# Kernel tuning notes

Hardware: AMD Instinct MI355X
Metric: run time of the kernel (lower is better)

The kernel has to match this reference:

```python
import jax, jax.numpy as jnp
import numpy as np

N_NODES = 50000
N_EDGES = 400000
N_GRAPHS = 128
IN_DIM = 768
HID = 128
N_CLASSES = 11
BN_EPS = 1e-5


def _sage_conv(x, src, dst, Wl, bl, Wr):
    # PyG SAGEConv (aggr='mean'): out = lin_l(mean_{j->i} x_j) + lin_r(x_i)
    # messages flow src -> dst; nodes with no in-edges get a zero aggregate.
    n = x.shape[0]
    deg = jax.ops.segment_sum(jnp.ones_like(dst, x.dtype), dst, num_segments=n)
    agg = jax.ops.segment_sum(x[src], dst, num_segments=n)  # [N, d] gather+scatter
    agg = agg / jnp.maximum(deg, 1.0)[:, None]
    return agg @ Wl.T + bl + x @ Wr.T


def _batch_norm(x, gamma, beta):
    # training-mode BatchNorm1d: biased batch statistics over the node axis
    m = jnp.mean(x, axis=0)
    v = jnp.var(x, axis=0)
    return (x - m) * jax.lax.rsqrt(v + BN_EPS) * gamma + beta


def setup_inputs() -> dict:
    key = jax.random.key(0)
    ks = jax.random.split(key, 16)
    x = jax.random.normal(ks[0], (N_NODES, IN_DIM), dtype=jnp.float32)
    edge_index = jax.random.randint(ks[1], (2, N_EDGES), 0, N_NODES, dtype=jnp.int32)
    batch = jnp.sort(jax.random.randint(ks[2], (N_NODES,), 0, N_GRAPHS, dtype=jnp.int32))

    def lin_w(k, out_d, in_d):
        return jax.random.normal(k, (out_d, in_d), dtype=jnp.float32) * (1.0 / np.sqrt(in_d))

    params = {
        'W1l': lin_w(ks[3], HID, IN_DIM), 'b1': jnp.zeros((HID,), jnp.float32),
        'W1r': lin_w(ks[4], HID, IN_DIM),
        'g1': jnp.ones((HID,), jnp.float32), 'be1': jnp.zeros((HID,), jnp.float32),
        'W2l': lin_w(ks[5], HID, HID), 'b2': jnp.zeros((HID,), jnp.float32),
        'W2r': lin_w(ks[6], HID, HID),
        'g2': jnp.ones((HID,), jnp.float32), 'be2': jnp.zeros((HID,), jnp.float32),
        'W3l': lin_w(ks[7], HID, HID), 'b3': jnp.zeros((HID,), jnp.float32),
        'W3r': lin_w(ks[8], HID, HID),
        'g3': jnp.ones((HID,), jnp.float32), 'be3': jnp.zeros((HID,), jnp.float32),
        'Wlin': lin_w(ks[9], N_CLASSES, HID), 'blin': jnp.zeros((N_CLASSES,), jnp.float32),
    }
    return {'x': x, 'edge_index': edge_index, 'batch': batch, **params}


def reference(x, edge_index, batch,
              W1l, b1, W1r, g1, be1,
              W2l, b2, W2r, g2, be2,
              W3l, b3, W3r, g3, be3,
              Wlin, blin):
    src, dst = edge_index[0], edge_index[1]
    h = jax.nn.relu(_batch_norm(_sage_conv(x, src, dst, W1l, b1, W1r), g1, be1))
    h = jax.nn.relu(_batch_norm(_sage_conv(h, src, dst, W2l, b2, W2r), g2, be2))
    h = _batch_norm(_sage_conv(h, src, dst, W3l, b3, W3r), g3, be3)
    # global_max_pool over graph ids
    pooled = jax.ops.segment_max(h, batch, num_segments=N_GRAPHS)  # [G, HID]
    # dropout is identity at inference
    return pooled @ Wlin.T + blin  # [G, 11]
```

## Files before the change

### kernel.cpp

```cpp
#include <hip/hip_runtime.h>

#define N_NODESC 50000
#define N_EDGESC 400000
#define N_GRAPHSC 128
#define IN_DIMC 768
#define HIDC 128
#define NCLSC 11
#define BN_EPSC 1e-5f
#define NB_AGG 8
#define NREP 64
#define SCAN_NB ((N_NODESC + 255) / 256)

typedef __bf16 bf16_t;
typedef __bf16 bf16x2 __attribute__((ext_vector_type(2)));
typedef __bf16 bf16x8 __attribute__((ext_vector_type(8)));
typedef float f32x4 __attribute__((ext_vector_type(4)));

typedef __attribute__((address_space(1))) void glb_void;
typedef __attribute__((address_space(3))) void lds_void;

__device__ __forceinline__ void cp16(const void* g, void* l) {
    __builtin_amdgcn_global_load_lds((glb_void*)g, (lds_void*)l, 16, 0, 0);
}

__device__ __forceinline__ f32x4 mfma_16x16x32_bf16(bf16x8 a, bf16x8 b, f32x4 c) {
    return __builtin_amdgcn_mfma_f32_16x16x32_bf16(a, b, c, 0, 0, 0);
}

template<int MODE, int KC>
__global__ __launch_bounds__(256) void gemm_kernel(const void* __restrict__ Av,
                                                   const bf16_t* __restrict__ Wb,
                                                   const float* __restrict__ stats,
                                                   const float* __restrict__ g,
                                                   const float* __restrict__ be,
                                                   bf16_t* __restrict__ Cl,
                                                   bf16_t* __restrict__ Cr,
                                                   int M)
{
    constexpr int NK   = KC / 32;
    constexpr int ASZ  = 8192;
    constexpr int BSZ  = 8192;
    constexpr int SCSZ = (MODE == 1) ? 1024 : 16;
    __shared__ __align__(16) unsigned char smem[3 * ASZ + 3 * BSZ + SCSZ];
    unsigned char* Asm = smem;
    unsigned char* Bsm = smem + 3 * ASZ;
    float* scS = (float*)(smem + 3 * ASZ + 3 * BSZ);

    const int bid  = blockIdx.x;
    const int p    = ((bid >> 4) << 3) + (bid & 7);
    const int half = (bid >> 3) & 1;
    if (p * 128 >= M) return;
    const int m0 = p * 128;

    const int t    = threadIdx.x;
    const int wid  = t >> 6;
    const int lane = t & 63;
    const int wm   = (wid >> 1) * 64;
    const int wn   = (wid & 1) * 64;
    const int l16  = lane & 15;
    const int quad = lane >> 4;

    const char* bSrc[2]; int bDst[2];
#pragma unroll
    for (int s = 0; s < 2; s++) {
        int L = (s * 4 + wid) * 64 + lane;
        int r = L >> 2;
        int c = (L & 3) ^ ((r >> 1) & 3);
        bSrc[s] = (const char*)(Wb + (size_t)(half * 128 + r) * KC + c * 8);
        bDst[s] = (s * 4 + wid) * 1024;
    }

    const char* aSrc[2]; int aDst[2];
    if constexpr (MODE == 1) {
#pragma unroll
        for (int s = 0; s < 2; s++) {
            int L = (s * 4 + wid) * 64 + lane;
            int r = L >> 2;
            int c = (L & 3) ^ ((r >> 1) & 3);
            int row = m0 + r; if (row > M - 1) row = M - 1;
            aSrc[s] = (const char*)Av + ((size_t)row * KC + (size_t)c * 8) * 2;
            aDst[s] = (s * 4 + wid) * 1024;
        }
    }

    const int rL = (wid << 5) + (lane >> 1);
    int rAg = m0 + rL; if (rAg > M - 1) rAg = M - 1;
    const int hA = lane & 1;
    const float* aG = (const float*)Av + (size_t)rAg * KC + hA * 16;
    const int cA0 = hA * 2;
    const int wb0 = rL * 64 + (((cA0)     ^ ((rL >> 1) & 3)) << 4);
    const int wb1 = rL * 64 + (((cA0 + 1) ^ ((rL >> 1) & 3)) << 4);

    int aOff[4], bOff[4];
#pragma unroll
    for (int i = 0; i < 4; i++) {
        int ra = wm + i * 16 + l16;
        aOff[i] = ra * 64 + ((quad ^ ((ra >> 1) & 3)) << 4);
        int rb = wn + i * 16 + l16;
        bOff[i] = rb * 64 + ((quad ^ ((rb >> 1) & 3)) << 4);
    }

    if (MODE == 1) {
        if (t < HIDC) {
            float sum = 0.f, sumsq = 0.f;
            for (int r = 0; r < NREP; r++) {
                sum   += stats[r * 256 + t];
                sumsq += stats[r * 256 + HIDC + t];
            }
            float invM = 1.0f / (float)M;
            float mean = sum * invM;
            float var  = sumsq * invM - mean * mean;
            float s = rsqrtf(var + BN_EPSC) * g[t];
            scS[t] = s;
            scS[HIDC + t] = be[t] - mean * s;
        }
        __syncthreads();
    }

    f32x4 acc[4][4] = {};

#define ALD(IT, G0, G1, G2, G3) { \
        const float4* _p = (const float4*)(aG + (size_t)(IT) * 32); \
        G0 = _p[0]; G1 = _p[1]; G2 = _p[2]; G3 = _p[3]; }
#define CVTW(G0, G1, G2, G3, DST) { \
        bf16x8 _w0, _w1; \
        _w0[0]=(bf16_t)G0.x; _w0[1]=(bf16_t)G0.y; _w0[2]=(bf16_t)G0.z; _w0[3]=(bf16_t)G0.w; \
        _w0[4]=(bf16_t)G1.x; _w0[5]=(bf16_t)G1.y; _w0[6]=(bf16_t)G1.z; _w0[7]=(bf16_t)G1.w; \
        _w1[0]=(bf16_t)G2.x; _w1[1]=(bf16_t)G2.y; _w1[2]=(bf16_t)G2.z; _w1[3]=(bf16_t)G2.w; \
        _w1[4]=(bf16_t)G3.x; _w1[5]=(bf16_t)G3.y; _w1[6]=(bf16_t)G3.z; _w1[7]=(bf16_t)G3.w; \
        *(bf16x8*)((DST) + wb0) = _w0; *(bf16x8*)((DST) + wb1) = _w1; }

    if constexpr (MODE == 0) {
        float4 gaA0, gaA1, gaA2, gaA3;
        float4 gaB0, gaB1, gaB2, gaB3;

        ALD(0, gaA0, gaA1, gaA2, gaA3);
#pragma unroll
        for (int s = 0; s < 2; s++) cp16(bSrc[s], Bsm + bDst[s]);
        ALD(1, gaB0, gaB1, gaB2, gaB3);
#pragma unroll
        for (int s = 0; s < 2; s++) cp16(bSrc[s] + 64, Bsm + BSZ + bDst[s]);
        CVTW(gaA0, gaA1, gaA2, gaA3, Asm);

        for (int it = 0; it < NK; ++it) {
            if (it + 1 < NK) asm volatile("s_waitcnt vmcnt(6) lgkmcnt(0)" ::: "memory");
            else             asm volatile("s_waitcnt vmcnt(0) lgkmcnt(0)" ::: "memory");
            asm volatile("s_barrier" ::: "memory");

            if (it + 2 < NK) {
                const size_t kb = (size_t)(it + 2) * 64;
                const int nb = (it + 2) % 3;
#pragma unroll
                for (int s = 0; s < 2; s++) cp16(bSrc[s] + kb, Bsm + nb * BSZ + bDst[s]);
                if ((it & 1) == 0) { ALD(it + 2, gaA0, gaA1, gaA2, gaA3); }
                else               { ALD(it + 2, gaB0, gaB1, gaB2, gaB3); }
            }
            if (it + 1 < NK) {
                unsigned char* Ad = Asm + ((it + 1) % 3) * ASZ;
                if ((it & 1) == 0) { CVTW(gaB0, gaB1, gaB2, gaB3, Ad); }
                else               { CVTW(gaA0, gaA1, gaA2, gaA3, Ad); }
            }

            const unsigned char* Ab = Asm + (it % 3) * ASZ;
            const unsigned char* Bb = Bsm + (it % 3) * BSZ;
            bf16x8 af[4], bfr[4];
#pragma unroll
            for (int i = 0; i < 4; i++)
                af[i] = *(const bf16x8*)(Ab + aOff[i]);
#pragma unroll
            for (int j = 0; j < 4; j++)
                bfr[j] = *(const bf16x8*)(Bb + bOff[j]);
#pragma unroll
            for (int i = 0; i < 4; i++)
#pragma unroll
                for (int j = 0; j < 4; j++)
                    acc[i][j] = mfma_16x16x32_bf16(af[i], bfr[j], acc[i][j]);
        }
    } else {
#pragma unroll
        for (int s = 0; s < 2; s++) cp16(aSrc[s], Asm + aDst[s]);
#pragma unroll
        for (int s = 0; s < 2; s++) cp16(bSrc[s], Bsm + bDst[s]);
#pragma unroll
        for (int s = 0; s < 2; s++) cp16(aSrc[s] + 64, Asm + ASZ + aDst[s]);
#pragma unroll
        for (int s = 0; s < 2; s++) cp16(bSrc[s] + 64, Bsm + BSZ + bDst[s]);

        for (int it = 0; it < NK; ++it) {
            if (it + 2 < NK) {
                const size_t kb2 = (size_t)(it + 2) * 64;
                const int nb = (it + 2) % 3;
#pragma unroll
                for (int s = 0; s < 2; s++) cp16(aSrc[s] + kb2, Asm + nb * ASZ + aDst[s]);
#pragma unroll
                for (int s = 0; s < 2; s++) cp16(bSrc[s] + kb2, Bsm + nb * BSZ + bDst[s]);
                asm volatile("s_waitcnt vmcnt(8)" ::: "memory");
            } else if (it + 1 < NK) {
                asm volatile("s_waitcnt vmcnt(4)" ::: "memory");
            } else {
                asm volatile("s_waitcnt vmcnt(0)" ::: "memory");
            }
            asm volatile("s_barrier" ::: "memory");

            const unsigned char* Ab = Asm + (it % 3) * ASZ;
            const unsigned char* Bb = Bsm + (it % 3) * BSZ;
            bf16x8 af[4], bfr[4];
            float4 s0 = *(const float4*)&scS[it * 32 + quad * 8];
            float4 s1 = *(const float4*)&scS[it * 32 + quad * 8 + 4];
            float4 h0 = *(const float4*)&scS[HIDC + it * 32 + quad * 8];
            float4 h1 = *(const float4*)&scS[HIDC + it * 32 + quad * 8 + 4];
            float ss[8] = {s0.x, s0.y, s0.z, s0.w, s1.x, s1.y, s1.z, s1.w};
            float hh[8] = {h0.x, h0.y, h0.z, h0.w, h1.x, h1.y, h1.z, h1.w};
#pragma unroll
            for (int i = 0; i < 4; i++) {
                bf16x8 raw = *(const bf16x8*)(Ab + aOff[i]);
#pragma unroll
                for (int e = 0; e < 8; e++)
                    af[i][e] = (bf16_t)fmaxf(fmaf((float)raw[e], ss[e], hh[e]), 0.0f);
            }
#pragma unroll
            for (int j = 0; j < 4; j++)
                bfr[j] = *(const bf16x8*)(Bb + bOff[j]);
#pragma unroll
            for (int i = 0; i < 4; i++)
#pragma unroll
                for (int j = 0; j < 4; j++)
                    acc[i][j] = mfma_16x16x32_bf16(af[i], bfr[j], acc[i][j]);

            asm volatile("s_barrier" ::: "memory");
        }
    }
#undef ALD
#undef CVTW

    bf16_t* C = half ? Cr : Cl;
#pragma unroll
    for (int i = 0; i < 4; i++) {
        int rowb = m0 + wm + i * 16 + quad * 4;
#pragma unroll
        for (int j = 0; j < 4; j++) {
            int colh = wn + j * 16 + l16;
#pragma unroll
            for (int rr = 0; rr < 4; rr++) {
                int row = rowb + rr;
                if (row < M) C[(size_t)row * HIDC + colh] = (bf16_t)acc[i][j][rr];
            }
        }
    }
}

__global__ void init_kernel(const float* __restrict__ W1l, const float* __restrict__ W1r,
                            const float* __restrict__ W2l, const float* __restrict__ W2r,
                            const float* __restrict__ W3l, const float* __restrict__ W3r,
                            bf16_t* __restrict__ Wb1, bf16_t* __restrict__ Wb2,
                            bf16_t* __restrict__ Wb3,
                            int* __restrict__ degi, float* __restrict__ stats)
{
    const int NW1 = 128 * IN_DIMC;
    const int NW2 = 128 * HIDC;
    const int NS  = 3 * NREP * 256;
    int j = blockIdx.x * blockDim.x + threadIdx.x;
    if (j < 2 * NW1) { Wb1[j] = (bf16_t)((j < NW1) ? W1l[j] : W1r[j - NW1]); return; }
    j -= 2 * NW1;
    if (j < 2 * NW2) { Wb2[j] = (bf16_t)((j < NW2) ? W2l[j] : W2r[j - NW2]); return; }
    j -= 2 * NW2;
    if (j < 2 * NW2) { Wb3[j] = (bf16_t)((j < NW2) ? W3l[j] : W3r[j - NW2]); return; }
    j -= 2 * NW2;
    if (j < NS) { stats[j] = 0.0f; return; }
    j -= NS;
    if (j < N_NODESC) degi[j] = 0;
}

__global__ void degi_kernel(const int* __restrict__ ei, int* __restrict__ degi) {
    int e = blockIdx.x * blockDim.x + threadIdx.x;
    if (e < N_EDGESC) atomicAdd(&degi[ei[N_EDGESC + e]], 1);
}

__global__ __launch_bounds__(256) void scan1_kernel(const int* __restrict__ degi,
                                                    int* __restrict__ local,
                                                    int* __restrict__ partials)
{
    __shared__ int tmp[256];
    const int t = threadIdx.x;
    const int i = blockIdx.x * 256 + t;
    int v = (i < N_NODESC) ? degi[i] : 0;
    tmp[t] = v;
    __syncthreads();
    for (int off = 1; off < 256; off <<= 1) {
        int u = (t >= off) ? tmp[t - off] : 0;
        __syncthreads();
        tmp[t] += u;
        __syncthreads();
    }
    if (i < N_NODESC) local[i] = tmp[t] - v;
    if (t == 255) partials[blockIdx.x] = tmp[255];
}

__global__ __launch_bounds__(256) void scan3_kernel(const int* __restrict__ local,
                                                    const int* __restrict__ partials,
                                                    int* __restrict__ rowptr,
                                                    int* __restrict__ cursor)
{
    __shared__ int inc[256];
    __shared__ int orig[256];
    const int t = threadIdx.x;
    int v = (t < SCAN_NB) ? partials[t] : 0;
    inc[t] = v; orig[t] = v;
    __syncthreads();
    for (int off = 1; off < 256; off <<= 1) {
        int u = (t >= off) ? inc[t - off] : 0;
        __syncthreads();
        inc[t] += u;
        __syncthreads();
    }
    const int boff = inc[blockIdx.x] - orig[blockIdx.x];
    const int i = blockIdx.x * 256 + t;
    if (i < N_NODESC) {
        int r = local[i] + boff;
        rowptr[i] = r;
        cursor[i] = r;
    }
    if (i == 0) rowptr[N_NODESC] = N_EDGESC;
}

__global__ void fill_kernel(const int* __restrict__ ei, int* __restrict__ cursor,
                            int* __restrict__ col) {
    int e = blockIdx.x * blockDim.x + threadIdx.x;
    if (e >= N_EDGESC) return;
    int d = ei[N_EDGESC + e];
    int pos = atomicAdd(&cursor[d], 1);
    col[pos] = ei[e];
}

__global__ __launch_bounds__(128) void agg_combine_kernel(const int* __restrict__ rowptr,
                                                          const int* __restrict__ col,
                                                          const bf16_t* __restrict__ Plb,
                                                          const bf16_t* __restrict__ Prb,
                                                          const float* __restrict__ bias,
                                                          bf16_t* __restrict__ Hb,
                                                          float* __restrict__ stats, int M)
{
    const int lane = threadIdx.x & 63;
    const int wv   = threadIdx.x >> 6;
    const int c0   = lane * 2;
    const float b0 = bias[c0], b1v = bias[c0 + 1];
    float s0 = 0.f, s1 = 0.f, q0 = 0.f, q1 = 0.f;
    const int n0 = blockIdx.x * NB_AGG + wv * (NB_AGG / 2);
    for (int rr = 0; rr < NB_AGG / 2; rr++) {
        int n = n0 + rr;
        if (n >= M) break;
        int lo = rowptr[n], hi = rowptr[n + 1];
        float a0 = 0.f, a1 = 0.f;
        for (int e = lo; e < hi; e += 8) {
            int rem = hi - e;
            int idx[8];
#pragma unroll
            for (int j = 0; j < 8; j++) {
                int ee = e + j; if (ee > hi - 1) ee = hi - 1;
                idx[j] = col[ee];
            }
            bf16x2 v[8];
#pragma unroll
            for (int j = 0; j < 8; j++)
                v[j] = *(const bf16x2*)&Plb[(size_t)idx[j] * HIDC + c0];
#pragma unroll
            for (int j = 0; j < 8; j++)
                if (j < rem) { a0 += (float)v[j][0]; a1 += (float)v[j][1]; }
        }
        int d = hi - lo;
        float inv = 1.0f / (float)(d > 0 ? d : 1);
        bf16x2 pr = *(const bf16x2*)&Prb[(size_t)n * HIDC + c0];
        float pre0 = fmaf(a0, inv, b0) + (float)pr[0];
        float pre1 = fmaf(a1, inv, b1v) + (float)pr[1];
        bf16x2 hv; hv[0] = (bf16_t)pre0; hv[1] = (bf16_t)pre1;
        *(bf16x2*)&Hb[(size_t)n * HIDC + c0] = hv;
        s0 += pre0; s1 += pre1; q0 += pre0 * pre0; q1 += pre1 * pre1;
    }
    const int rep = (blockIdx.x * 2 + wv) & (NREP - 1);
    atomicAdd(&stats[rep * 256 + c0], s0);
    atomicAdd(&stats[rep * 256 + c0 + 1], s1);
    atomicAdd(&stats[rep * 256 + HIDC + c0], q0);
    atomicAdd(&stats[rep * 256 + HIDC + c0 + 1], q1);
}

__global__ __launch_bounds__(128) void poolhead_kernel(const bf16_t* __restrict__ Hb,
                                                       const float* __restrict__ stats,
                                                       const float* __restrict__ g,
                                                       const float* __restrict__ be,
                                                       const int* __restrict__ batch,
                                                       const float* __restrict__ Wlin,
                                                       const float* __restrict__ blin,
                                                       float* __restrict__ out, int M)
{
    __shared__ float sp[HIDC];
    int gph = blockIdx.x;
    int c   = threadIdx.x;
    float sum = 0.f, sumsq = 0.f;
    for (int r = 0; r < NREP; r++) {
        sum   += stats[r * 256 + c];
        sumsq += stats[r * 256 + HIDC + c];
    }
    float invM = 1.0f / (float)M;
    float mean = sum * invM;
    float var  = sumsq * invM - mean * mean;
    float s = rsqrtf(var + BN_EPSC) * g[c];
    float h = be[c] - mean * s;

    int lo = 0, hi = M;
    while (lo < hi) { int m = (lo + hi) >> 1; if (batch[m] < gph) lo = m + 1; else hi = m; }
    int lo2 = lo, hi2 = M;
    while (lo2 < hi2) { int m = (lo2 + hi2) >> 1; if (batch[m] < gph + 1) lo2 = m + 1; else hi2 = m; }
    float mx = -INFINITY;
    for (int rr = lo; rr < lo2; rr++)
        mx = fmaxf(mx, fmaf((float)Hb[(size_t)rr * HIDC + c], s, h));
    sp[c] = mx;
    __syncthreads();
    if (c < NCLSC) {
        float acc = blin[c];
        for (int k = 0; k < HIDC; k++) acc += sp[k] * Wlin[c * HIDC + k];
        out[gph * NCLSC + c] = acc;
    }
}

extern "C" void kernel_launch(void* const* d_in, const int* in_sizes, int n_in,
                              void* d_out, int out_size, void* d_ws, size_t ws_size,
                              hipStream_t stream)
{
    const float* x     = (const float*)d_in[0];
    const int*   ei    = (const int*)d_in[1];
    const int*   batch = (const int*)d_in[2];
    const float* W1l = (const float*)d_in[3];
    const float* b1  = (const float*)d_in[4];
    const float* W1r = (const float*)d_in[5];
    const float* g1  = (const float*)d_in[6];
    const float* be1 = (const float*)d_in[7];
    const float* W2l = (const float*)d_in[8];
    const float* b2  = (const float*)d_in[9];
    const float* W2r = (const float*)d_in[10];
    const float* g2  = (const float*)d_in[11];
    const float* be2 = (const float*)d_in[12];
    const float* W3l = (const float*)d_in[13];
    const float* b3  = (const float*)d_in[14];
    const float* W3r = (const float*)d_in[15];
    const float* g3  = (const float*)d_in[16];
    const float* be3 = (const float*)d_in[17];
    const float* Wlin = (const float*)d_in[18];
    const float* blin = (const float*)d_in[19];

    const int M = N_NODESC;

    char* w = (char*)d_ws;
    bf16_t* Plb  = (bf16_t*)w;  w += (size_t)M * HIDC * 2;
    bf16_t* Prb  = (bf16_t*)w;  w += (size_t)M * HIDC * 2;
    bf16_t* Hb   = (bf16_t*)w;  w += (size_t)M * HIDC * 2;
    bf16_t* Wb1  = (bf16_t*)w;  w += (size_t)256 * IN_DIMC * 2;
    bf16_t* Wb2  = (bf16_t*)w;  w += (size_t)256 * HIDC * 2;
    bf16_t* Wb3  = (bf16_t*)w;  w += (size_t)256 * HIDC * 2;
    int*   rowptr= (int*)w;     w += (size_t)(M + 16) * 4;
    int*   col   = (int*)w;     w += (size_t)N_EDGESC * 4;
    int*   cursor= (int*)w;     w += (size_t)M * 4;
    int*   degi  = (int*)w;     w += (size_t)M * 4;
    int*   slocal= (int*)w;     w += (size_t)M * 4;
    int*   spart = (int*)w;     w += 256 * 4;
    float* stats = (float*)w;   w += (size_t)3 * NREP * 256 * 4;

    float* stats1 = stats;
    float* stats2 = stats + NREP * 256;
    float* stats3 = stats + 2 * NREP * 256;

    const int nP = (M + 127) / 128;
    const dim3 gemm_grid(((nP + 7) / 8) * 16);
    const int agg_blocks = (M + NB_AGG - 1) / NB_AGG;
    const int init_total = 2 * 128 * IN_DIMC + 4 * 128 * HIDC + 3 * NREP * 256 + M;

    init_kernel<<<(init_total + 255) / 256, 256, 0, stream>>>(W1l, W1r, W2l, W2r, W3l, W3r,
                                                              Wb1, Wb2, Wb3, degi, stats);
    degi_kernel<<<(N_EDGESC + 255) / 256, 256, 0, stream>>>(ei, degi);
    scan1_kernel<<<SCAN_NB, 256, 0, stream>>>(degi, slocal, spart);
    scan3_kernel<<<SCAN_NB, 256, 0, stream>>>(slocal, spart, rowptr, cursor);
    fill_kernel<<<(N_EDGESC + 255) / 256, 256, 0, stream>>>(ei, cursor, col);

    gemm_kernel<0, IN_DIMC><<<gemm_grid, 256, 0, stream>>>(x, Wb1, nullptr, nullptr, nullptr,
                                                           Plb, Prb, M);
    agg_combine_kernel<<<agg_blocks, 128, 0, stream>>>(rowptr, col, Plb, Prb, b1, Hb, stats1, M);

    gemm_kernel<1, HIDC><<<gemm_grid, 256, 0, stream>>>(Hb, Wb2, stats1, g1, be1, Plb, Prb, M);
    agg_combine_kernel<<<agg_blocks, 128, 0, stream>>>(rowptr, col, Plb, Prb, b2, Hb, stats2, M);

    gemm_kernel<1, HIDC><<<gemm_grid, 256, 0, stream>>>(Hb, Wb3, stats2, g2, be2, Plb, Prb, M);
    agg_combine_kernel<<<agg_blocks, 128, 0, stream>>>(rowptr, col, Plb, Prb, b3, Hb, stats3, M);

    poolhead_kernel<<<N_GRAPHSC, 128, 0, stream>>>(Hb, stats3, g3, be3, batch, Wlin, blin,
                                                   (float*)d_out, M);
}
```

Baseline: 593.4 us.

## Load fp32 A operand directly into MFMA fragments, bypassing LDS staging

In the first-layer GEMM (MODE 0), each lane now loads the fp32 A rows it needs for its MFMA fragments straight from global memory into registers and converts them to bf16 there. This replaces the previous scheme of cooperative global loads, conversion and LDS writes followed by LDS reads. The A staging buffers are dropped from shared memory, which cuts LDS traffic and shared-memory footprint and may raise occupancy. The cost is redundant global loads: the two wave columns each re-read the same A rows, and the new loads are less coalesced (32-byte chunks per lane). Register pressure also rises, and a second barrier per iteration is added.

```diff
diff --git a/kernel.cpp b/kernel.cpp
--- a/kernel.cpp
+++ b/kernel.cpp
@@ -41,10 +41,11 @@
     constexpr int ASZ  = 8192;
     constexpr int BSZ  = 8192;
     constexpr int SCSZ = (MODE == 1) ? 1024 : 16;
-    __shared__ __align__(16) unsigned char smem[3 * ASZ + 3 * BSZ + SCSZ];
+    constexpr int SMSZ = ((MODE == 0) ? 3 * BSZ : 3 * ASZ + 3 * BSZ) + SCSZ;
+    __shared__ __align__(16) unsigned char smem[SMSZ];
     unsigned char* Asm = smem;
-    unsigned char* Bsm = smem + 3 * ASZ;
-    float* scS = (float*)(smem + 3 * ASZ + 3 * BSZ);
+    unsigned char* Bsm = (MODE == 0) ? smem : smem + 3 * ASZ;
+    float* scS = (float*)(smem + SMSZ - SCSZ);
 
     const int bid  = blockIdx.x;
     const int p    = ((bid >> 4) << 3) + (bid & 7);
@@ -83,21 +84,22 @@
         }
     }
 
-    const int rL = (wid << 5) + (lane >> 1);
-    int rAg = m0 + rL; if (rAg > M - 1) rAg = M - 1;
-    const int hA = lane & 1;
-    const float* aG = (const float*)Av + (size_t)rAg * KC + hA * 16;
-    const int cA0 = hA * 2;
-    const int wb0 = rL * 64 + (((cA0)     ^ ((rL >> 1) & 3)) << 4);
-    const int wb1 = rL * 64 + (((cA0 + 1) ^ ((rL >> 1) & 3)) << 4);
+    const float* aG[4];
+    if constexpr (MODE == 0) {
+#pragma unroll
+        for (int i = 0; i < 4; i++) {
+            int r = m0 + wm + i * 16 + l16; if (r > M - 1) r = M - 1;
+            aG[i] = (const float*)Av + (size_t)r * KC + quad * 8;
+        }
+    }
 
     int aOff[4], bOff[4];
 #pragma unroll
     for (int i = 0; i < 4; i++) {
         int ra = wm + i * 16 + l16;
-        aOff[i] = ra * 64 + ((quad ^ ((ra >> 1) & 3)) << 4);
+        aOff[i] = ra * 64 + ((quad ^ ((ra >> 1) & 3)) * 16);
         int rb = wn + i * 16 + l16;
-        bOff[i] = rb * 64 + ((quad ^ ((rb >> 1) & 3)) << 4);
+        bOff[i] = rb * 64 + ((quad ^ ((rb >> 1) & 3)) * 16);
     }
 
     if (MODE == 1) {
@@ -119,54 +121,66 @@
 
     f32x4 acc[4][4] = {};
 
-#define ALD(IT, G0, G1, G2, G3) { \
-        const float4* _p = (const float4*)(aG + (size_t)(IT) * 32); \
-        G0 = _p[0]; G1 = _p[1]; G2 = _p[2]; G3 = _p[3]; }
-#define CVTW(G0, G1, G2, G3, DST) { \
-        bf16x8 _w0, _w1; \
-        _w0[0]=(bf16_t)G0.x; _w0[1]=(bf16_t)G0.y; _w0[2]=(bf16_t)G0.z; _w0[3]=(bf16_t)G0.w; \
-        _w0[4]=(bf16_t)G1.x; _w0[5]=(bf16_t)G1.y; _w0[6]=(bf16_t)G1.z; _w0[7]=(bf16_t)G1.w; \
-        _w1[0]=(bf16_t)G2.x; _w1[1]=(bf16_t)G2.y; _w1[2]=(bf16_t)G2.z; _w1[3]=(bf16_t)G2.w; \
-        _w1[4]=(bf16_t)G3.x; _w1[5]=(bf16_t)G3.y; _w1[6]=(bf16_t)G3.z; _w1[7]=(bf16_t)G3.w; \
-        *(bf16x8*)((DST) + wb0) = _w0; *(bf16x8*)((DST) + wb1) = _w1; }
-
     if constexpr (MODE == 0) {
-        float4 gaA0, gaA1, gaA2, gaA3;
-        float4 gaB0, gaB1, gaB2, gaB3;
-
-        ALD(0, gaA0, gaA1, gaA2, gaA3);
+        float4 aEv[4][2], aOd[4][2];
+
 #pragma unroll
         for (int s = 0; s < 2; s++) cp16(bSrc[s], Bsm + bDst[s]);
-        ALD(1, gaB0, gaB1, gaB2, gaB3);
+#pragma unroll
+        for (int i = 0; i < 4; i++) {
+            aEv[i][0] = *(const float4*)(aG[i]);
+            aEv[i][1] = *(const float4*)(aG[i] + 4);
+        }
 #pragma unroll
         for (int s = 0; s < 2; s++) cp16(bSrc[s] + 64, Bsm + BSZ + bDst[s]);
-        CVTW(gaA0, gaA1, gaA2, gaA3, Asm);
 
         for (int it = 0; it < NK; ++it) {
-            if (it + 1 < NK) asm volatile("s_waitcnt vmcnt(6) lgkmcnt(0)" ::: "memory");
-            else             asm volatile("s_waitcnt vmcnt(0) lgkmcnt(0)" ::: "memory");
-            asm volatile("s_barrier" ::: "memory");
-
             if (it + 2 < NK) {
                 const size_t kb = (size_t)(it + 2) * 64;
                 const int nb = (it + 2) % 3;
 #pragma unroll
                 for (int s = 0; s < 2; s++) cp16(bSrc[s] + kb, Bsm + nb * BSZ + bDst[s]);
-                if ((it & 1) == 0) { ALD(it + 2, gaA0, gaA1, gaA2, gaA3); }
-                else               { ALD(it + 2, gaB0, gaB1, gaB2, gaB3); }
             }
             if (it + 1 < NK) {
-                unsigned char* Ad = Asm + ((it + 1) % 3) * ASZ;
-                if ((it & 1) == 0) { CVTW(gaB0, gaB1, gaB2, gaB3, Ad); }
-                else               { CVTW(gaA0, gaA1, gaA2, gaA3, Ad); }
-            }
-
-            const unsigned char* Ab = Asm + (it % 3) * ASZ;
+                const size_t ka = (size_t)(it + 1) * 32;
+                if ((it & 1) == 0) {
+#pragma unroll
+                    for (int i = 0; i < 4; i++) {
+                        aOd[i][0] = *(const float4*)(aG[i] + ka);
+                        aOd[i][1] = *(const float4*)(aG[i] + ka + 4);
+                    }
+                } else {
+#pragma unroll
+                    for (int i = 0; i < 4; i++) {
+                        aEv[i][0] = *(const float4*)(aG[i] + ka);
+                        aEv[i][1] = *(const float4*)(aG[i] + ka + 4);
+                    }
+                }
+            }
+            if (it + 2 < NK)      asm volatile("s_waitcnt vmcnt(20)" ::: "memory");
+            else if (it + 1 < NK) asm volatile("s_waitcnt vmcnt(18)" ::: "memory");
+            else                  asm volatile("s_waitcnt vmcnt(0)"  ::: "memory");
+            asm volatile("s_barrier" ::: "memory");
+
+            bf16x8 af[4], bfr[4];
+            if ((it & 1) == 0) {
+#pragma unroll
+                for (int i = 0; i < 4; i++) {
+                    af[i][0] = (bf16_t)aEv[i][0].x; af[i][1] = (bf16_t)aEv[i][0].y;
+                    af[i][2] = (bf16_t)aEv[i][0].z; af[i][3] = (bf16_t)aEv[i][0].w;
+                    af[i][4] = (bf16_t)aEv[i][1].x; af[i][5] = (bf16_t)aEv[i][1].y;
+                    af[i][6] = (bf16_t)aEv[i][1].z; af[i][7] = (bf16_t)aEv[i][1].w;
+                }
+            } else {
+#pragma unroll
+                for (int i = 0; i < 4; i++) {
+                    af[i][0] = (bf16_t)aOd[i][0].x; af[i][1] = (bf16_t)aOd[i][0].y;
+                    af[i][2] = (bf16_t)aOd[i][0].z; af[i][3] = (bf16_t)aOd[i][0].w;
+                    af[i][4] = (bf16_t)aOd[i][1].x; af[i][5] = (bf16_t)aOd[i][1].y;
+                    af[i][6] = (bf16_t)aOd[i][1].z; af[i][7] = (bf16_t)aOd[i][1].w;
+                }
+            }
             const unsigned char* Bb = Bsm + (it % 3) * BSZ;
-            bf16x8 af[4], bfr[4];
-#pragma unroll
-            for (int i = 0; i < 4; i++)
-                af[i] = *(const bf16x8*)(Ab + aOff[i]);
 #pragma unroll
             for (int j = 0; j < 4; j++)
                 bfr[j] = *(const bf16x8*)(Bb + bOff[j]);
@@ -175,6 +189,8 @@
 #pragma unroll
                 for (int j = 0; j < 4; j++)
                     acc[i][j] = mfma_16x16x32_bf16(af[i], bfr[j], acc[i][j]);
+
+            asm volatile("s_barrier" ::: "memory");
         }
     } else {
 #pragma unroll
@@ -230,8 +246,6 @@
             asm volatile("s_barrier" ::: "memory");
         }
     }
-#undef ALD
-#undef CVTW
 
     bf16_t* C = half ? Cr : Cl;
 #pragma unroll
```

New measurement: 622.5 us. +4.9%, slower.
